# Optimization experiments

Hardware: AMD Instinct MI355X
Metric: run time of the kernel (lower is better)

Reference implementation:

```python
import jax, jax.numpy as jnp
import numpy as np

HIDDEN = 32
ODE_H = 0.1      # rk4 fixed step size (torchdiffeq options step_size=0.1)
ODE_STEPS = 10   # integrate t in [0, 1]


def gcn_conv(x, W, b, edge_index, n):
    """PyG GCNConv: symmetric norm with self-loops; x' = D^-1/2 (A+I) D^-1/2 (x W) + b."""
    h = x @ W                                  # [n, out]
    src, dst = edge_index[0], edge_index[1]
    deg = jnp.ones((n,), h.dtype).at[dst].add(1.0)   # +1 for self-loop
    dinv = jax.lax.rsqrt(deg)
    coef = (dinv[src] * dinv[dst])[:, None]
    agg = jnp.zeros_like(h).at[dst].add(h[src] * coef)
    agg = agg + h * (dinv * dinv)[:, None]     # self-loop term
    return agg + b


def ode_rk4(x0, edge_index, Wg, bg, wt, n):
    """RK4 integration of psi(t,x)=relu(GCN(x)) * sigmoid(t * wt) from t=0 to 1."""
    def f(t, x):
        gate = jax.nn.sigmoid(t * wt)          # [hidden], Linear(1,h,no bias).sigmoid()
        return jax.nn.relu(gcn_conv(x, Wg, bg, edge_index, n)) * gate

    h = ODE_H
    def step(x, t):
        k1 = f(t, x)
        k2 = f(t + h * 0.5, x + (h * 0.5) * k1)
        k3 = f(t + h * 0.5, x + (h * 0.5) * k2)
        k4 = f(t + h, x + h * k3)
        return x + (h / 6.0) * (k1 + 2.0 * k2 + 2.0 * k3 + k4), None

    ts = jnp.arange(ODE_STEPS, dtype=x0.dtype) * h
    xf, _ = jax.lax.scan(step, x0, ts)
    return xf


def setup_inputs() -> dict:
    key = jax.random.key(0)
    ks = jax.random.split(key, 16)
    N, IN, H = 100000, 128, HIDDEN
    E, DE = 1600000, 800000

    inp = {
        "H_t": jax.random.normal(ks[0], (N, IN), jnp.float32),
        "A_pos_t": jax.random.randint(ks[1], (2, E), 0, N),
        "A_neg_t": jax.random.randint(ks[2], (2, E), 0, N),
        "dA_pos": jax.random.randint(ks[3], (2, DE), 0, N),
        "dA_neg": jax.random.randint(ks[4], (2, DE), 0, N),
        # init GCN
        "W_init": jax.random.normal(ks[5], (IN, H), jnp.float32) / np.sqrt(IN),
        "b_init": jnp.zeros((H,), jnp.float32),
        # pos ODE func
        "W_pos": jax.random.normal(ks[6], (H, H), jnp.float32) / np.sqrt(H),
        "b_pos": jnp.zeros((H,), jnp.float32),
        "wt_pos": jax.random.normal(ks[7], (H,), jnp.float32),
        # neg ODE func
        "W_neg": jax.random.normal(ks[8], (H, H), jnp.float32) / np.sqrt(H),
        "b_neg": jnp.zeros((H,), jnp.float32),
        "wt_neg": jax.random.normal(ks[9], (H,), jnp.float32),
        # combine + layernorm
        "W_comb": jax.random.normal(ks[10], (2 * H, H), jnp.float32) / np.sqrt(2 * H),
        "b_comb": jnp.zeros((H,), jnp.float32),
        "ln_g": jnp.ones((H,), jnp.float32),
        "ln_b": jnp.zeros((H,), jnp.float32),
    }
    return inp


def reference(H_t, A_pos_t, A_neg_t, dA_pos, dA_neg,
              W_init, b_init, W_pos, b_pos, wt_pos,
              W_neg, b_neg, wt_neg, W_comb, b_comb, ln_g, ln_b):
    n = H_t.shape[0]
    edges_all = jnp.concatenate([A_pos_t, A_neg_t], axis=1)
    H = jax.nn.relu(gcn_conv(H_t, W_init, b_init, edges_all, n))   # [n, hidden]
    Z_pos = ode_rk4(H, dA_pos, W_pos, b_pos, wt_pos, n)
    Z_neg = ode_rk4(H, dA_neg, W_neg, b_neg, wt_neg, n)
    Z = jnp.concatenate([Z_pos, Z_neg], axis=-1) @ W_comb + b_comb # [n, hidden]
    mu = jnp.mean(Z, axis=-1, keepdims=True)
    var = jnp.var(Z, axis=-1, keepdims=True)
    return (Z - mu) * jax.lax.rsqrt(var + 1e-5) * ln_g + ln_b
```

## Files before the change

kernel.cpp:

```cpp
#include <hip/hip_runtime.h>
#include <math.h>


#define TPB 256
#define SCAN_T 1024
#define RB 512
#define PA_TILE 4096

typedef _Float16 h8 __attribute__((ext_vector_type(8)));
typedef float f8 __attribute__((ext_vector_type(8)));


struct SegG { const int* src; const int* dst; int n; int goff; };
struct FSeg { const int* src; const int* dst; int n; const int* offs; int* cur; };

__global__ void count4(SegG s0, SegG s1, SegG s2, SegG s3, int* __restrict__ cnt3) {
    int i = blockIdx.x * blockDim.x + threadIdx.x;
    SegG s; int e;
    if (i < s0.n) { s = s0; e = i; }
    else if (i < s0.n + s1.n) { s = s1; e = i - s0.n; }
    else if (i < s0.n + s1.n + s2.n) { s = s2; e = i - s0.n - s1.n; }
    else if (i < s0.n + s1.n + s2.n + s3.n) { s = s3; e = i - s0.n - s1.n - s2.n; }
    else return;
    atomicAdd(&cnt3[s.goff + s.dst[e]], 1);
}

__global__ void fill4(FSeg s0, FSeg s1, FSeg s2, FSeg s3, int* __restrict__ csr) {
    int i = blockIdx.x * blockDim.x + threadIdx.x;
    FSeg s; int e;
    if (i < s0.n) { s = s0; e = i; }
    else if (i < s0.n + s1.n) { s = s1; e = i - s0.n; }
    else if (i < s0.n + s1.n + s2.n) { s = s2; e = i - s0.n - s1.n; }
    else if (i < s0.n + s1.n + s2.n + s3.n) { s = s3; e = i - s0.n - s1.n - s2.n; }
    else return;
    int d = s.dst[e];
    int pos = s.offs[d] + atomicAdd(&s.cur[d], 1);
    csr[pos] = s.src[e];
}

__global__ void dinv_from_cnt(const int* __restrict__ cnt, float* __restrict__ dinv, int n) {
    int i = blockIdx.x * blockDim.x + threadIdx.x;
    if (i < n) dinv[i] = rsqrtf(1.0f + (float)cnt[i]);
}

__global__ void scan_block(const int* __restrict__ in, int n, int* __restrict__ out,
                           int* __restrict__ bsums) {
    __shared__ int sh[SCAN_T];
    int tx = threadIdx.x;
    int g = blockIdx.x * SCAN_T + tx;
    int v = (g < n) ? in[g] : 0;
    sh[tx] = v;
    __syncthreads();
    for (int off = 1; off < SCAN_T; off <<= 1) {
        int t = (tx >= off) ? sh[tx - off] : 0;
        __syncthreads();
        sh[tx] += t;
        __syncthreads();
    }
    if (g < n) out[g] = sh[tx] - v;
    if (tx == SCAN_T - 1) bsums[blockIdx.x] = sh[tx];
}

__global__ void scan_sums(int* __restrict__ bsums, int nb) {
    __shared__ int sh[SCAN_T];
    int tx = threadIdx.x;
    int v = (tx < nb) ? bsums[tx] : 0;
    sh[tx] = v;
    __syncthreads();
    for (int off = 1; off < SCAN_T; off <<= 1) {
        int t = (tx >= off) ? sh[tx - off] : 0;
        __syncthreads();
        sh[tx] += t;
        __syncthreads();
    }
    if (tx < nb) bsums[tx] = sh[tx] - v;
}

__global__ void scan_add(int* __restrict__ offs, const int* __restrict__ bsums, int n, int total) {
    int g = blockIdx.x * blockDim.x + threadIdx.x;
    if (g < n) offs[g] += bsums[g >> 10];
    if (g == 0) offs[n] = total;
}

__global__ void init_stage_cur(const int* __restrict__ offs3, int* __restrict__ stage_cur,
                               int B, int n3) {
    int b = blockIdx.x * blockDim.x + threadIdx.x;
    if (b < B) {
        int k = b << 10; if (k > n3) k = n3;
        stage_cur[b] = offs3[k];
    }
}

__global__ __launch_bounds__(TPB) void passA(SegG s0, SegG s1, SegG s2, SegG s3,
                                             int* __restrict__ stage_cur,
                                             int* __restrict__ staging, int Etot) {
    __shared__ int lh[RB];
    __shared__ int lbase[RB];
    int tid = threadIdx.x;
    int base = blockIdx.x * PA_TILE;
    int t1 = s0.n, t2 = t1 + s1.n, t3 = t2 + s2.n;

    for (int b = tid; b < RB; b += TPB) lh[b] = 0;
    __syncthreads();

    int gds[16], srcs[16];
#pragma unroll
    for (int k = 0; k < 16; ++k) {
        int i = base + k * TPB + tid;
        gds[k] = -1;
        if (i < Etot) {
            SegG s; int e;
            if (i < t1) { s = s0; e = i; }
            else if (i < t2) { s = s1; e = i - t1; }
            else if (i < t3) { s = s2; e = i - t2; }
            else { s = s3; e = i - t3; }
            int gd = s.goff + s.dst[e];
            gds[k] = gd;
            srcs[k] = s.src[e];
            atomicAdd(&lh[gd >> 10], 1);
        }
    }
    __syncthreads();
    for (int b = tid; b < RB; b += TPB) {
        int c = lh[b];
        lbase[b] = c ? atomicAdd(&stage_cur[b], c) : 0;
    }
    __syncthreads();
    for (int b = tid; b < RB; b += TPB) lh[b] = 0;
    __syncthreads();
#pragma unroll
    for (int k = 0; k < 16; ++k) {
        int gd = gds[k];
        if (gd >= 0) {
            int b = gd >> 10;
            int r = atomicAdd(&lh[b], 1);
            staging[lbase[b] + r] = ((gd & 1023) << 17) | srcs[k];
        }
    }
}

__global__ __launch_bounds__(TPB) void passB(const int* __restrict__ staging,
                                             const int* __restrict__ offs3,
                                             int* __restrict__ cur3,
                                             int* __restrict__ csr3, int n3) {
    int b = blockIdx.x >> 3, sl = blockIdx.x & 7;
    int k0 = b << 10;
    int k1 = k0 + 1024; if (k1 > n3) k1 = n3;
    if (k0 >= n3) return;
    int lo = offs3[k0], hi = offs3[k1];
    int len = hi - lo;
    int c0 = lo + (int)((long long)len * sl / 8);
    int c1 = lo + (int)((long long)len * (sl + 1) / 8);
    for (int i = c0 + threadIdx.x; i < c1; i += TPB) {
        int ent = staging[i];
        int gd = k0 + (ent >> 17);
        int pos = offs3[gd] + atomicAdd(&cur3[gd], 1);
        csr3[pos] = ent & 0x1FFFF;
    }
}


__global__ void mm32_kernel(const float* __restrict__ x, const float* __restrict__ W,
                            const float* __restrict__ dinv, _Float16* __restrict__ hs, int N) {
    __shared__ float Ws[32][32];
    __shared__ float xs[8][32];
    int tid = threadIdx.x;
    for (int i = tid; i < 32 * 32; i += TPB) Ws[i >> 5][i & 31] = W[i];
    int base = blockIdx.x * 8;
    {
        int idx = base * 32 + tid;
        xs[tid >> 5][tid & 31] = (idx < N * 32) ? x[idx] : 0.0f;
    }
    __syncthreads();
    int row = tid >> 5, c = tid & 31;
    int gr = base + row;
    float acc = 0.0f;
#pragma unroll
    for (int k = 0; k < 32; ++k) acc += xs[row][k] * Ws[k][c];
    if (gr < N) hs[gr * 32 + c] = (_Float16)(acc * dinv[gr]);
}

__global__ void mm128_kernel(const float* __restrict__ x, const float* __restrict__ W,
                             const float* __restrict__ dinv, _Float16* __restrict__ hs, int N) {
    __shared__ float Ws[128][32];
    __shared__ float xs[8][128];
    int tid = threadIdx.x;
    for (int i = tid; i < 128 * 32; i += TPB) Ws[i >> 5][i & 31] = W[i];
    int base = blockIdx.x * 8;
    for (int i = tid; i < 8 * 128; i += TPB) {
        int idx = base * 128 + i;
        xs[i >> 7][i & 127] = (idx < N * 128) ? x[idx] : 0.0f;
    }
    __syncthreads();
    int row = tid >> 5, c = tid & 31;
    int gr = base + row;
    float acc = 0.0f;
#pragma unroll
    for (int k = 0; k < 128; ++k) acc += xs[row][k] * Ws[k][c];
    if (gr < N) hs[gr * 32 + c] = (_Float16)(acc * dinv[gr]);
}


struct Job {
    const int* offs; const int* csr;
    const _Float16* hs_in; _Float16* hs_out;
    const float* dinv; const float* dinv_next;
    const float* bias; const float* wt;
    float* ksum; float* x;
    const float* W;
};

__global__ __launch_bounds__(TPB) void agg_stage(Job jp, Job jn, int nbp, float t,
                                                 int stage, int do_mm, float* __restrict__ x2,
                                                 int N) {
    __shared__ float Ws[32][32];
    __shared__ float xts[64][36];
    __shared__ int soffs[65];

    bool isP = blockIdx.x < nbp;
    const Job& J = isP ? jp : jn;
    int bid = isP ? blockIdx.x : (blockIdx.x - nbp);
    int nbase = bid * 64;
    int tid = threadIdx.x;
    int lnode = tid >> 2, q = tid & 3;
    int node = nbase + lnode;
    bool valid = node < N;

    if (do_mm) {
        for (int i = tid; i < 32 * 32; i += TPB) Ws[i >> 5][i & 31] = J.W[i];
    }
    if (tid < 65) {
        int ix = nbase + tid; if (ix > N) ix = N;
        soffs[tid] = J.offs[ix];
    }
    __syncthreads();

    f8 xrow;
#pragma unroll
    for (int j = 0; j < 8; ++j) xrow[j] = 0.f;

    if (valid) {
        const h8* hsv = (const h8*)J.hs_in;
        const int* __restrict__ csr = J.csr;
        int r0 = soffs[lnode], r1 = soffs[lnode + 1];
        f8 acc = __builtin_convertvector(hsv[node * 4 + q], f8);
        int i = r0;
        for (; i + 4 <= r1; i += 4) {
            int s0 = csr[i], s1 = csr[i + 1], s2 = csr[i + 2], s3 = csr[i + 3];
            h8 v0 = hsv[s0 * 4 + q];
            h8 v1 = hsv[s1 * 4 + q];
            h8 v2 = hsv[s2 * 4 + q];
            h8 v3 = hsv[s3 * 4 + q];
            acc += (__builtin_convertvector(v0, f8) + __builtin_convertvector(v1, f8))
                 + (__builtin_convertvector(v2, f8) + __builtin_convertvector(v3, f8));
        }
        for (; i < r1; ++i)
            acc += __builtin_convertvector(hsv[csr[i] * 4 + q], f8);

        float dv = J.dinv[node];
        f8 bb = ((const f8*)J.bias)[q];
        f8 kv;
#pragma unroll
        for (int j = 0; j < 8; ++j) kv[j] = fmaxf(acc[j] * dv + bb[j], 0.f);
        if (J.wt) {
            f8 w = ((const f8*)J.wt)[q];
#pragma unroll
            for (int j = 0; j < 8; ++j) kv[j] *= 1.f / (1.f + expf(-t * w[j]));
        }
        int idx = node * 4 + q;
        f8* x8 = (f8*)J.x;
        f8* ks8 = (f8*)J.ksum;
        if (stage == 0) {
            x8[idx] = kv;
            ((f8*)x2)[idx] = kv;
            xrow = kv;
        } else if (stage == 4) {
            f8 ks = ks8[idx];
            f8 xv = x8[idx];
            const float cc = 0.1f / 6.0f;
#pragma unroll
            for (int j = 0; j < 8; ++j) xv[j] += cc * (ks[j] + kv[j]);
            x8[idx] = xv;
            xrow = xv;
        } else {
            float a = (stage == 3) ? 0.1f : 0.05f;
            f8 xv = x8[idx];
#pragma unroll
            for (int j = 0; j < 8; ++j) xrow[j] = xv[j] + a * kv[j];
            if (stage == 1) {
                ks8[idx] = kv;
            } else {
                f8 ks = ks8[idx];
#pragma unroll
                for (int j = 0; j < 8; ++j) ks[j] += 2.f * kv[j];
                ks8[idx] = ks;
            }
        }
    }

    if (do_mm) {
        if (valid) {
#pragma unroll
            for (int j = 0; j < 8; ++j) xts[lnode][q * 8 + j] = xrow[j];
        }
        __syncthreads();
        if (valid) {
            f8 accm;
#pragma unroll
            for (int j = 0; j < 8; ++j) accm[j] = 0.f;
#pragma unroll
            for (int k = 0; k < 32; ++k) {
                float xv = xts[lnode][k];
                f8 w = *(const f8*)&Ws[k][q * 8];
                accm += xv * w;
            }
            accm *= J.dinv_next[node];
            ((h8*)J.hs_out)[node * 4 + q] = __builtin_convertvector(accm, h8);
        }
    }
}


__global__ void combine_kernel(const float* __restrict__ zp, const float* __restrict__ zn,
                               const float* __restrict__ Wc, const float* __restrict__ bc,
                               const float* __restrict__ g, const float* __restrict__ be,
                               float* __restrict__ out, int N) {
    __shared__ float Ws[64][32];
    __shared__ float zs[8][64];
    int tid = threadIdx.x;
    for (int i = tid; i < 64 * 32; i += TPB) Ws[i >> 5][i & 31] = Wc[i];
    int base = blockIdx.x * 8;
    {
        int r = tid >> 5, c = tid & 31;
        int gr = base + r;
        zs[r][c] = (gr < N) ? zp[gr * 32 + c] : 0.0f;
        zs[r][32 + c] = (gr < N) ? zn[gr * 32 + c] : 0.0f;
    }
    __syncthreads();
    int row = tid >> 5, c = tid & 31;
    int gr = base + row;
    float acc = bc[c];
#pragma unroll
    for (int k = 0; k < 64; ++k) acc += zs[row][k] * Ws[k][c];
    float s = acc, sq = acc * acc;
#pragma unroll
    for (int off = 16; off; off >>= 1) {
        s += __shfl_xor(s, off, 32);
        sq += __shfl_xor(sq, off, 32);
    }
    float mu = s * (1.0f / 32.0f);
    float var = sq * (1.0f / 32.0f) - mu * mu;
    float y = (acc - mu) * rsqrtf(var + 1e-5f) * g[c] + be[c];
    if (gr < N) out[gr * 32 + c] = y;
}


extern "C" void kernel_launch(void* const* d_in, const int* in_sizes, int n_in,
                              void* d_out, int out_size, void* d_ws, size_t ws_size,
                              hipStream_t stream) {
    const float* H_t = (const float*)d_in[0];
    const int* Apos = (const int*)d_in[1];
    const int* Aneg = (const int*)d_in[2];
    const int* dApos = (const int*)d_in[3];
    const int* dAneg = (const int*)d_in[4];
    const float* W_init = (const float*)d_in[5];
    const float* b_init = (const float*)d_in[6];
    const float* W_pos = (const float*)d_in[7];
    const float* b_pos = (const float*)d_in[8];
    const float* wt_pos = (const float*)d_in[9];
    const float* W_neg = (const float*)d_in[10];
    const float* b_neg = (const float*)d_in[11];
    const float* wt_neg = (const float*)d_in[12];
    const float* W_comb = (const float*)d_in[13];
    const float* b_comb = (const float*)d_in[14];
    const float* ln_g = (const float*)d_in[15];
    const float* ln_b = (const float*)d_in[16];

    const int N = in_sizes[0] / 128;
    const int E1 = in_sizes[1] / 2;
    const int E2 = in_sizes[2] / 2;
    const int DE1 = in_sizes[3] / 2;
    const int DE2 = in_sizes[4] / 2;
    const int Etot = E1 + E2 + DE1 + DE2;

    const int* Apos_src = Apos, * Apos_dst = Apos + E1;
    const int* Aneg_src = Aneg, * Aneg_dst = Aneg + E2;
    const int* dApos_src = dApos, * dApos_dst = dApos + DE1;
    const int* dAneg_src = dAneg, * dAneg_dst = dAneg + DE2;

    const size_t n32 = (size_t)N * 32;
    const size_t szf = n32 * 4;
    const size_t szh = n32 * 2;
    auto al = [](size_t b) { return (b + 255) & ~(size_t)255; };

    size_t small_bytes = 3 * al((size_t)(3 * N) * 4)
                       + al((3 * (size_t)N + 1) * 4)
                       + al((size_t)Etot * 4)
                       + al(SCAN_T * 4);
    size_t need_merged = 4 * al(szf) + 4 * al(szh) + small_bytes;
    size_t need_radix = need_merged + al((size_t)Etot * 4) + al(RB * 4);
    bool merged = ws_size >= need_merged + 4096;
    bool radix = merged && (ws_size >= need_radix + 4096) && (N <= 131071)
                 && (((3 * N + 1023) >> 10) <= RB);

    char* p = (char*)d_ws;
    auto alloc = [&](size_t bytes) -> void* {
        void* r = (void*)p;
        p += al(bytes);
        return r;
    };
    float* x_pos = (float*)alloc(szf);
    float* x_neg = (float*)alloc(szf);
    float* ksum_p = (float*)alloc(szf);
    float* ksum_n = merged ? (float*)alloc(szf) : ksum_p;
    _Float16* hs_pa = (_Float16*)alloc(szh);
    _Float16* hs_pb = (_Float16*)alloc(szh);
    _Float16* hs_na = merged ? (_Float16*)alloc(szh) : hs_pa;
    _Float16* hs_nb = merged ? (_Float16*)alloc(szh) : hs_pb;
    float* dinv3 = (float*)alloc((size_t)(3 * N) * 4);
    int* cnt3 = (int*)alloc((size_t)(3 * N) * 4);
    int* cur3 = (int*)alloc((size_t)(3 * N) * 4);
    int* offs3 = (int*)alloc((3 * (size_t)N + 1) * 4);
    int* csr3 = (int*)alloc((size_t)Etot * 4);
    int* bsums = (int*)alloc(SCAN_T * 4);
    int* staging = radix ? (int*)alloc((size_t)Etot * 4) : nullptr;
    int* stage_cur = radix ? (int*)alloc(RB * 4) : nullptr;

    size_t used = (size_t)(p - (char*)d_ws);
    if (used > ws_size) used = ws_size;

    hipMemsetAsync(d_ws, 0, used, stream);

    float* dinv_all = dinv3, * dinv_pos = dinv3 + N, * dinv_neg = dinv3 + 2 * N;
    const int* offs_all = offs3, * offs_pos = offs3 + N, * offs_neg = offs3 + 2 * N;

    dim3 blk(TPB);
    auto gblk = [](int n) { return dim3((n + TPB - 1) / TPB); };
    dim3 grid_rows((N + 7) / 8);
    const int nb64 = (N + 63) / 64;
    const int n3 = 3 * N;
    const int nbs = (n3 + SCAN_T - 1) / SCAN_T;
    const int B = (n3 + 1023) >> 10;

    SegG s0 = { Apos_src, Apos_dst, E1, 0 };
    SegG s1 = { Aneg_src, Aneg_dst, E2, 0 };
    SegG s2 = { dApos_src, dApos_dst, DE1, N };
    SegG s3 = { dAneg_src, dAneg_dst, DE2, 2 * N };
    count4<<<gblk(Etot), blk, 0, stream>>>(s0, s1, s2, s3, cnt3);
    dinv_from_cnt<<<gblk(n3), blk, 0, stream>>>(cnt3, dinv3, n3);
    scan_block<<<nbs, SCAN_T, 0, stream>>>(cnt3, n3, offs3, bsums);
    scan_sums<<<1, SCAN_T, 0, stream>>>(bsums, nbs);
    scan_add<<<gblk(n3), blk, 0, stream>>>(offs3, bsums, n3, Etot);
    if (radix) {
        init_stage_cur<<<gblk(B), blk, 0, stream>>>(offs3, stage_cur, B, n3);
        passA<<<(Etot + PA_TILE - 1) / PA_TILE, blk, 0, stream>>>(s0, s1, s2, s3,
                                                                  stage_cur, staging, Etot);
        passB<<<B * 8, blk, 0, stream>>>(staging, offs3, cur3, csr3, n3);
    } else {
        FSeg f0 = { Apos_src, Apos_dst, E1, offs3, cur3 };
        FSeg f1 = { Aneg_src, Aneg_dst, E2, offs3, cur3 };
        FSeg f2 = { dApos_src, dApos_dst, DE1, offs3 + N, cur3 + N };
        FSeg f3 = { dAneg_src, dAneg_dst, DE2, offs3 + 2 * N, cur3 + 2 * N };
        fill4<<<gblk(Etot), blk, 0, stream>>>(f0, f1, f2, f3, csr3);
    }

    auto mkjob = [&](const int* offs, const _Float16* hs_in, _Float16* hs_out,
                     const float* dinv, const float* dinv_next, const float* bias,
                     const float* wt, float* ksum, float* x, const float* W) {
        Job j; j.offs = offs; j.csr = csr3; j.hs_in = hs_in; j.hs_out = hs_out;
        j.dinv = dinv; j.dinv_next = dinv_next; j.bias = bias; j.wt = wt;
        j.ksum = ksum; j.x = x; j.W = W; return j;
    };

    mm128_kernel<<<grid_rows, blk, 0, stream>>>(H_t, W_init, dinv_all, hs_pa, N);
    {
        Job j0 = mkjob(offs_all, hs_pa, hs_pb, dinv_all, dinv_pos, b_init,
                       nullptr, nullptr, x_pos, W_pos);
        agg_stage<<<nb64, blk, 0, stream>>>(j0, j0, nb64, 0.0f, 0, 1, x_neg, N);
    }

    if (merged) {
        mm32_kernel<<<grid_rows, blk, 0, stream>>>(x_neg, W_neg, dinv_neg, hs_nb, N);
        for (int s = 0; s < 10; ++s) {
            float t0 = 0.1f * (float)s;
            int last_mm = (s == 9) ? 0 : 1;
            Job p1 = mkjob(offs_pos, hs_pb, hs_pa, dinv_pos, dinv_pos, b_pos, wt_pos, ksum_p, x_pos, W_pos);
            Job n1 = mkjob(offs_neg, hs_nb, hs_na, dinv_neg, dinv_neg, b_neg, wt_neg, ksum_n, x_neg, W_neg);
            agg_stage<<<2 * nb64, blk, 0, stream>>>(p1, n1, nb64, t0, 1, 1, nullptr, N);
            Job p2 = p1; p2.hs_in = hs_pa; p2.hs_out = hs_pb;
            Job n2 = n1; n2.hs_in = hs_na; n2.hs_out = hs_nb;
            agg_stage<<<2 * nb64, blk, 0, stream>>>(p2, n2, nb64, t0 + 0.05f, 2, 1, nullptr, N);
            agg_stage<<<2 * nb64, blk, 0, stream>>>(p1, n1, nb64, t0 + 0.05f, 3, 1, nullptr, N);
            agg_stage<<<2 * nb64, blk, 0, stream>>>(p2, n2, nb64, t0 + 0.1f, 4, last_mm, nullptr, N);
        }
    } else {
        for (int ode = 0; ode < 2; ++ode) {
            float* x = ode ? x_neg : x_pos;
            const float* W = ode ? W_neg : W_pos;
            const float* b = ode ? b_neg : b_pos;
            const float* wt = ode ? wt_neg : wt_pos;
            const float* dinv = ode ? dinv_neg : dinv_pos;
            const int* offs = ode ? offs_neg : offs_pos;
            if (ode == 1) {
                mm32_kernel<<<grid_rows, blk, 0, stream>>>(x, W, dinv, hs_pb, N);
            }
            for (int s = 0; s < 10; ++s) {
                float t0 = 0.1f * (float)s;
                int last_mm = (s == 9) ? 0 : 1;
                Job j1 = mkjob(offs, hs_pb, hs_pa, dinv, dinv, b, wt, ksum_p, x, W);
                Job j2 = j1; j2.hs_in = hs_pa; j2.hs_out = hs_pb;
                agg_stage<<<nb64, blk, 0, stream>>>(j1, j1, nb64, t0, 1, 1, nullptr, N);
                agg_stage<<<nb64, blk, 0, stream>>>(j2, j2, nb64, t0 + 0.05f, 2, 1, nullptr, N);
                agg_stage<<<nb64, blk, 0, stream>>>(j1, j1, nb64, t0 + 0.05f, 3, 1, nullptr, N);
                agg_stage<<<nb64, blk, 0, stream>>>(j2, j2, nb64, t0 + 0.1f, 4, last_mm, nullptr, N);
            }
        }
    }

    combine_kernel<<<grid_rows, blk, 0, stream>>>(x_pos, x_neg, W_comb, b_comb, ln_g, ln_b,
                                                  (float*)d_out, N);
}
```

Baseline: 2.325 ms.

## Replace per-stage ODE launches with persistent kernel using global barrier

Replaces the 40 agg_stage launches of the RK4 loop with one persistent kernel of 512 blocks. The blocks split between the positive and negative ODE, keep x and the RK4 partial sums (fp16) resident in shared memory, and synchronise through a two-level atomic grid barrier. The radix-based CSR build (passA/passB) is removed and the simple atomic fill path is used instead. This cuts launch overhead and global traffic for x and ksum, but it relies on all blocks being co-resident, stores the k sums in fp16, and may make the CSR build slower.

```diff
diff --git a/kernel.cpp b/kernel.cpp
--- a/kernel.cpp
+++ b/kernel.cpp
@@ -4,10 +4,14 @@
 
 #define TPB 256
 #define SCAN_T 1024
-#define RB 512
-#define PA_TILE 4096
+
+#define PB 512
+#define PNB 392
+#define PGH 256
+#define PG 512
 
 typedef _Float16 h8 __attribute__((ext_vector_type(8)));
+typedef _Float16 h2v __attribute__((ext_vector_type(2)));
 typedef float f8 __attribute__((ext_vector_type(8)));
 
 
@@ -80,83 +84,6 @@
     int g = blockIdx.x * blockDim.x + threadIdx.x;
     if (g < n) offs[g] += bsums[g >> 10];
     if (g == 0) offs[n] = total;
-}
-
-__global__ void init_stage_cur(const int* __restrict__ offs3, int* __restrict__ stage_cur,
-                               int B, int n3) {
-    int b = blockIdx.x * blockDim.x + threadIdx.x;
-    if (b < B) {
-        int k = b << 10; if (k > n3) k = n3;
-        stage_cur[b] = offs3[k];
-    }
-}
-
-__global__ __launch_bounds__(TPB) void passA(SegG s0, SegG s1, SegG s2, SegG s3,
-                                             int* __restrict__ stage_cur,
-                                             int* __restrict__ staging, int Etot) {
-    __shared__ int lh[RB];
-    __shared__ int lbase[RB];
-    int tid = threadIdx.x;
-    int base = blockIdx.x * PA_TILE;
-    int t1 = s0.n, t2 = t1 + s1.n, t3 = t2 + s2.n;
-
-    for (int b = tid; b < RB; b += TPB) lh[b] = 0;
-    __syncthreads();
-
-    int gds[16], srcs[16];
-#pragma unroll
-    for (int k = 0; k < 16; ++k) {
-        int i = base + k * TPB + tid;
-        gds[k] = -1;
-        if (i < Etot) {
-            SegG s; int e;
-            if (i < t1) { s = s0; e = i; }
-            else if (i < t2) { s = s1; e = i - t1; }
-            else if (i < t3) { s = s2; e = i - t2; }
-            else { s = s3; e = i - t3; }
-            int gd = s.goff + s.dst[e];
-            gds[k] = gd;
-            srcs[k] = s.src[e];
-            atomicAdd(&lh[gd >> 10], 1);
-        }
-    }
-    __syncthreads();
-    for (int b = tid; b < RB; b += TPB) {
-        int c = lh[b];
-        lbase[b] = c ? atomicAdd(&stage_cur[b], c) : 0;
-    }
-    __syncthreads();
-    for (int b = tid; b < RB; b += TPB) lh[b] = 0;
-    __syncthreads();
-#pragma unroll
-    for (int k = 0; k < 16; ++k) {
-        int gd = gds[k];
-        if (gd >= 0) {
-            int b = gd >> 10;
-            int r = atomicAdd(&lh[b], 1);
-            staging[lbase[b] + r] = ((gd & 1023) << 17) | srcs[k];
-        }
-    }
-}
-
-__global__ __launch_bounds__(TPB) void passB(const int* __restrict__ staging,
-                                             const int* __restrict__ offs3,
-                                             int* __restrict__ cur3,
-                                             int* __restrict__ csr3, int n3) {
-    int b = blockIdx.x >> 3, sl = blockIdx.x & 7;
-    int k0 = b << 10;
-    int k1 = k0 + 1024; if (k1 > n3) k1 = n3;
-    if (k0 >= n3) return;
-    int lo = offs3[k0], hi = offs3[k1];
-    int len = hi - lo;
-    int c0 = lo + (int)((long long)len * sl / 8);
-    int c1 = lo + (int)((long long)len * (sl + 1) / 8);
-    for (int i = c0 + threadIdx.x; i < c1; i += TPB) {
-        int ent = staging[i];
-        int gd = k0 + (ent >> 17);
-        int pos = offs3[gd] + atomicAdd(&cur3[gd], 1);
-        csr3[pos] = ent & 0x1FFFF;
-    }
 }
 
 
@@ -316,6 +243,182 @@
             }
             accm *= J.dinv_next[node];
             ((h8*)J.hs_out)[node * 4 + q] = __builtin_convertvector(accm, h8);
+        }
+    }
+}
+
+__global__ __launch_bounds__(PB, 4) void ode_persistent(
+    const int* __restrict__ offs3, const int* __restrict__ csr3,
+    const float* __restrict__ dinv3,
+    _Float16* __restrict__ hp0, _Float16* __restrict__ hp1,
+    _Float16* __restrict__ hn0, _Float16* __restrict__ hn1,
+    const float* __restrict__ bp, const float* __restrict__ wtp, const float* __restrict__ Wp,
+    const float* __restrict__ bn, const float* __restrict__ wtn, const float* __restrict__ Wn,
+    float* __restrict__ x_pos, float* __restrict__ x_neg,
+    int* __restrict__ bar_leaf, int* __restrict__ bar_root, int N)
+{
+    __shared__ float xs[PNB][33];
+    __shared__ h2v  ks[PNB][16];
+    __shared__ float Wsh[32][32];
+
+    int tid = threadIdx.x;
+    bool isP = blockIdx.x < PGH;
+    int bid = isP ? blockIdx.x : (blockIdx.x - PGH);
+    int nbase = bid * PNB;
+    const int* offs = offs3 + (isP ? N : 2 * N);
+    const float* dinv = dinv3 + (isP ? (size_t)N : (size_t)2 * N);
+    const float* Wg = isP ? Wp : Wn;
+    const float* bg = isP ? bp : bn;
+    const float* wtg = isP ? wtp : wtn;
+    _Float16* buf0 = isP ? hp0 : hn0;
+    _Float16* buf1 = isP ? hp1 : hn1;
+    float* xg = isP ? x_pos : x_neg;
+
+    for (int i = tid; i < 32 * 32; i += PB) Wsh[i >> 5][i & 31] = Wg[i];
+
+    int lnode = tid >> 2, q = tid & 3;
+    f8 bb = ((const f8*)bg)[q];
+    f8 wv = ((const f8*)wtg)[q];
+
+    for (int c = 0; c < 4; ++c) {
+        int ln = c * 128 + lnode;
+        int node = nbase + ln;
+        if (ln < PNB && node < N) {
+            f8 xv = ((const f8*)xg)[node * 4 + q];
+#pragma unroll
+            for (int j = 0; j < 8; ++j) xs[ln][q * 8 + j] = xv[j];
+        }
+    }
+    __syncthreads();
+
+    for (int cc = 0; cc < 40; ++cc) {
+        int step = cc >> 2;
+        int st = (cc & 3) + 1;
+        float t = 0.1f * (float)step + ((st == 1) ? 0.f : (st == 4) ? 0.1f : 0.05f);
+        const _Float16* hin = (cc & 1) ? buf1 : buf0;
+        _Float16* hout = (cc & 1) ? buf0 : buf1;
+        bool do_mm = (cc != 39);
+
+        f8 gate;
+#pragma unroll
+        for (int j = 0; j < 8; ++j) gate[j] = 1.f / (1.f + expf(-t * wv[j]));
+
+        for (int c = 0; c < 4; ++c) {
+            int ln = c * 128 + lnode;
+            int node = nbase + ln;
+            bool v = (ln < PNB) && (node < N);
+            if (!v) continue;
+
+            const h8* hsv = (const h8*)hin;
+            int r0 = offs[node], r1 = offs[node + 1];
+            f8 acc = __builtin_convertvector(hsv[node * 4 + q], f8);
+            int i = r0;
+            for (; i + 4 <= r1; i += 4) {
+                int s0 = csr3[i], s1 = csr3[i + 1], s2 = csr3[i + 2], s3 = csr3[i + 3];
+                h8 v0 = hsv[s0 * 4 + q];
+                h8 v1 = hsv[s1 * 4 + q];
+                h8 v2 = hsv[s2 * 4 + q];
+                h8 v3 = hsv[s3 * 4 + q];
+                acc += (__builtin_convertvector(v0, f8) + __builtin_convertvector(v1, f8))
+                     + (__builtin_convertvector(v2, f8) + __builtin_convertvector(v3, f8));
+            }
+            for (; i < r1; ++i)
+                acc += __builtin_convertvector(hsv[csr3[i] * 4 + q], f8);
+
+            float dv = dinv[node];
+            f8 kv;
+#pragma unroll
+            for (int j = 0; j < 8; ++j)
+                kv[j] = fmaxf(acc[j] * dv + bb[j], 0.f) * gate[j];
+
+            f8 xv;
+#pragma unroll
+            for (int j = 0; j < 8; ++j) xv[j] = xs[ln][q * 8 + j];
+            f8 xrow;
+            if (st == 4) {
+                const float hc = 0.1f / 6.0f;
+#pragma unroll
+                for (int jj = 0; jj < 4; ++jj) {
+                    h2v kk = ks[ln][q * 4 + jj];
+                    xrow[2 * jj] = xv[2 * jj] + hc * ((float)kk[0] + kv[2 * jj]);
+                    xrow[2 * jj + 1] = xv[2 * jj + 1] + hc * ((float)kk[1] + kv[2 * jj + 1]);
+                }
+#pragma unroll
+                for (int j = 0; j < 8; ++j) xs[ln][q * 8 + j] = xrow[j];
+            } else {
+                float a = (st == 3) ? 0.1f : 0.05f;
+#pragma unroll
+                for (int j = 0; j < 8; ++j) xrow[j] = xv[j] + a * kv[j];
+                if (st == 1) {
+#pragma unroll
+                    for (int jj = 0; jj < 4; ++jj) {
+                        h2v kk;
+                        kk[0] = (_Float16)kv[2 * jj];
+                        kk[1] = (_Float16)kv[2 * jj + 1];
+                        ks[ln][q * 4 + jj] = kk;
+                    }
+                } else {
+#pragma unroll
+                    for (int jj = 0; jj < 4; ++jj) {
+                        h2v kk = ks[ln][q * 4 + jj];
+                        kk[0] = (_Float16)((float)kk[0] + 2.f * kv[2 * jj]);
+                        kk[1] = (_Float16)((float)kk[1] + 2.f * kv[2 * jj + 1]);
+                        ks[ln][q * 4 + jj] = kk;
+                    }
+                }
+            }
+
+            if (do_mm) {
+                float lo16[16];
+#pragma unroll
+                for (int j = 0; j < 8; ++j) {
+                    float o = __shfl_xor(xrow[j], 1, 64);
+                    lo16[j] = (q & 1) ? o : xrow[j];
+                    lo16[8 + j] = (q & 1) ? xrow[j] : o;
+                }
+                int base1 = (q & ~1) * 8;
+                int base2 = ((q ^ 2) & ~1) * 8;
+                f8 accm;
+#pragma unroll
+                for (int j = 0; j < 8; ++j) accm[j] = 0.f;
+#pragma unroll
+                for (int k = 0; k < 16; ++k)
+                    accm += lo16[k] * ((const f8*)&Wsh[base1 + k][0])[q];
+#pragma unroll
+                for (int k = 0; k < 16; ++k) {
+                    float o2 = __shfl_xor(lo16[k], 2, 64);
+                    accm += o2 * ((const f8*)&Wsh[base2 + k][0])[q];
+                }
+                accm *= dv;
+                ((h8*)hout)[node * 4 + q] = __builtin_convertvector(accm, h8);
+            }
+        }
+
+        if (cc != 39) {
+            __syncthreads();
+            if (tid == 0) {
+                __threadfence();
+                int leaf = blockIdx.x >> 3;
+                int old = atomicAdd(&bar_leaf[leaf], 1);
+                if ((old & 7) == 7) atomicAdd(bar_root, 1);
+                int target = 64 * (cc + 1);
+                while (__hip_atomic_load(bar_root, __ATOMIC_RELAXED,
+                                         __HIP_MEMORY_SCOPE_AGENT) < target)
+                    __builtin_amdgcn_s_sleep(8);
+                __threadfence();
+            }
+            __syncthreads();
+        }
+    }
+
+    for (int c = 0; c < 4; ++c) {
+        int ln = c * 128 + lnode;
+        int node = nbase + ln;
+        if (ln < PNB && node < N) {
+            f8 out;
+#pragma unroll
+            for (int j = 0; j < 8; ++j) out[j] = xs[ln][q * 8 + j];
+            ((f8*)xg)[node * 4 + q] = out;
         }
     }
 }
@@ -396,12 +499,10 @@
     size_t small_bytes = 3 * al((size_t)(3 * N) * 4)
                        + al((3 * (size_t)N + 1) * 4)
                        + al((size_t)Etot * 4)
-                       + al(SCAN_T * 4);
+                       + al(SCAN_T * 4) + al(65 * 4);
     size_t need_merged = 4 * al(szf) + 4 * al(szh) + small_bytes;
-    size_t need_radix = need_merged + al((size_t)Etot * 4) + al(RB * 4);
     bool merged = ws_size >= need_merged + 4096;
-    bool radix = merged && (ws_size >= need_radix + 4096) && (N <= 131071)
-                 && (((3 * N + 1023) >> 10) <= RB);
+    bool persistent = merged && (N <= PNB * PGH);
 
     char* p = (char*)d_ws;
     auto alloc = [&](size_t bytes) -> void* {
@@ -423,8 +524,7 @@
     int* offs3 = (int*)alloc((3 * (size_t)N + 1) * 4);
     int* csr3 = (int*)alloc((size_t)Etot * 4);
     int* bsums = (int*)alloc(SCAN_T * 4);
-    int* staging = radix ? (int*)alloc((size_t)Etot * 4) : nullptr;
-    int* stage_cur = radix ? (int*)alloc(RB * 4) : nullptr;
+    int* bar = (int*)alloc(65 * 4);
 
     size_t used = (size_t)(p - (char*)d_ws);
     if (used > ws_size) used = ws_size;
@@ -440,7 +540,6 @@
     const int nb64 = (N + 63) / 64;
     const int n3 = 3 * N;
     const int nbs = (n3 + SCAN_T - 1) / SCAN_T;
-    const int B = (n3 + 1023) >> 10;
 
     SegG s0 = { Apos_src, Apos_dst, E1, 0 };
     SegG s1 = { Aneg_src, Aneg_dst, E2, 0 };
@@ -451,12 +550,7 @@
     scan_block<<<nbs, SCAN_T, 0, stream>>>(cnt3, n3, offs3, bsums);
     scan_sums<<<1, SCAN_T, 0, stream>>>(bsums, nbs);
     scan_add<<<gblk(n3), blk, 0, stream>>>(offs3, bsums, n3, Etot);
-    if (radix) {
-        init_stage_cur<<<gblk(B), blk, 0, stream>>>(offs3, stage_cur, B, n3);
-        passA<<<(Etot + PA_TILE - 1) / PA_TILE, blk, 0, stream>>>(s0, s1, s2, s3,
-                                                                  stage_cur, staging, Etot);
-        passB<<<B * 8, blk, 0, stream>>>(staging, offs3, cur3, csr3, n3);
-    } else {
+    {
         FSeg f0 = { Apos_src, Apos_dst, E1, offs3, cur3 };
         FSeg f1 = { Aneg_src, Aneg_dst, E2, offs3, cur3 };
         FSeg f2 = { dApos_src, dApos_dst, DE1, offs3 + N, cur3 + N };
@@ -478,9 +572,15 @@
                        nullptr, nullptr, x_pos, W_pos);
         agg_stage<<<nb64, blk, 0, stream>>>(j0, j0, nb64, 0.0f, 0, 1, x_neg, N);
     }
-
-    if (merged) {
-        mm32_kernel<<<grid_rows, blk, 0, stream>>>(x_neg, W_neg, dinv_neg, hs_nb, N);
+    mm32_kernel<<<grid_rows, blk, 0, stream>>>(x_neg, W_neg, dinv_neg, hs_nb, N);
+
+    if (persistent) {
+        ode_persistent<<<PG, PB, 0, stream>>>(
+            offs3, csr3, dinv3,
+            hs_pb, hs_pa, hs_nb, hs_na,
+            b_pos, wt_pos, W_pos, b_neg, wt_neg, W_neg,
+            x_pos, x_neg, bar, bar + 64, N);
+    } else if (merged) {
         for (int s = 0; s < 10; ++s) {
             float t0 = 0.1f * (float)s;
             int last_mm = (s == 9) ? 0 : 1;
```

Result: slower. 2.989 ms (+28.6%).
